# Kernel tuning notes

Hardware: AMD Instinct MI355X
Metric: run time of the kernel (lower is better)

## Reference

```python
import jax, jax.numpy as jnp
import numpy as np

B, D, C = 524288, 8, 32
EPS = 1e-4
DT, BETA, CLAMP, STEPS = 0.12, 1.0, 3.0, 4


def setup_inputs() -> dict:
    key = jax.random.key(0)
    k1, k2 = jax.random.split(key)
    z = jax.random.normal(k1, (B, D), dtype=jnp.float32)
    centers = jax.random.normal(k2, (C, D), dtype=jnp.float32) * 0.7
    mus = jnp.ones((C,), dtype=jnp.float32) * 0.4
    return {"z": z, "centers": centers, "mus": mus}


def reference(z, centers, mus):
    def grad_ln_n(z):
        # rvec: (B, C, D)
        rvec = z[:, None, :] - centers[None, :, :]
        r2 = jnp.sum(rvec * rvec, axis=-1) + EPS   # (B, C)
        r = jnp.sqrt(r2)
        n = 1.0 + jnp.sum(mus[None, :] / r, axis=-1)          # (B,)
        # g = sum_c -mu_c * rvec_c / (r_c * r2_c)
        g = -jnp.sum((mus[None, :] / (r * r2))[:, :, None] * rvec, axis=1)  # (B, D)
        return g / n[:, None]

    for _ in range(STEPS):
        z = jnp.clip(z + DT * BETA * grad_ln_n(z), -CLAMP, CLAMP)
    return z
```

## Files before the change

kernel.cpp:

```cpp
#include <hip/hip_runtime.h>
#include <stdint.h>

#define NB 524288
#define NC 32
#define EPSV 1e-4f
#define DTB 0.12f
#define CLAMPV 3.0f
#define NSTEPS 4

typedef float f32x16 __attribute__((ext_vector_type(16)));
typedef short short8 __attribute__((ext_vector_type(8)));

union FragU { uint32_t u[4]; short8 s; uint4 q; };

__device__ __forceinline__ uint32_t pkbf16(float a, float b) {
    uint32_t r;
    asm("v_cvt_pk_bf16_f32 %0, %1, %2" : "=v"(r) : "v"(a), "v"(b));
    return r;
}
__device__ __forceinline__ float lo16f(uint32_t w) { return __uint_as_float(w << 16); }
__device__ __forceinline__ float hi16f(uint32_t w) { return __uint_as_float(w & 0xffff0000u); }
__device__ __forceinline__ float sx32(float v) { return __shfl_xor(v, 32); }

__global__ void prep_kernel(const float* __restrict__ centers,
                            const float* __restrict__ mus,
                            uint4* __restrict__ wsu) {
    int t = threadIdx.x;
    if (t >= 64) return;
    int row = t & 31, part = t >> 5;

    float mu = mus[row];
    float im2 = 1.0f / (mu * mu);
    float c[8];
    float bb = EPSV;
    #pragma unroll
    for (int d = 0; d < 8; ++d) { c[d] = centers[row * 8 + d]; bb = fmaf(c[d], c[d], bb); }
    float v[8];
    #pragma unroll
    for (int i = 0; i < 8; ++i) {
        int k = part * 8 + i;
        v[i] = (k < 8) ? (-2.0f * c[k] * im2) : (k == 8) ? (bb * im2) : 0.0f;
    }
    uint32_t h[4], l[4];
    #pragma unroll
    for (int j = 0; j < 4; ++j) {
        float a = v[2 * j], b = v[2 * j + 1];
        h[j] = pkbf16(a, b);
        l[j] = pkbf16(a - lo16f(h[j]), b - hi16f(h[j]));
    }
    wsu[t]      = make_uint4(h[0], h[1], h[2], h[3]);
    wsu[64 + t] = make_uint4(l[0], l[1], l[2], l[3]);

    #pragma unroll
    for (int ch = 0; ch < 2; ++ch) {
        float v2[8];
        #pragma unroll
        for (int i = 0; i < 8; ++i) {
            int k = part * 8 + i;
            int within = (k & 3) + 8 * ((k >> 2) & 1) + 4 * (k >> 3);
            int ci = ch * 16 + within;
            float muc = mus[ci];
            float im2c = 1.0f / (muc * muc);
            v2[i] = (row < 8) ? (centers[ci * 8 + row] * im2c) : (row == 8) ? im2c : 0.0f;
        }
        uint32_t h2[4], l2[4];
        #pragma unroll
        for (int j = 0; j < 4; ++j) {
            float a = v2[2 * j], b = v2[2 * j + 1];
            h2[j] = pkbf16(a, b);
            l2[j] = pkbf16(a - lo16f(h2[j]), b - hi16f(h2[j]));
        }
        wsu[128 + ch * 64 + t] = make_uint4(h2[0], h2[1], h2[2], h2[3]);
        wsu[256 + ch * 64 + t] = make_uint4(l2[0], l2[1], l2[2], l2[3]);
    }

    if (t < 32) {
        int h2i = t >> 4, r = t & 15;
        int ci = (r & 3) + 8 * (r >> 2) + 4 * h2i;
        float muc = mus[ci];
        ((float*)wsu)[1536 + t] = 1.0f / (muc * muc);
    }
}

__global__ __launch_bounds__(256, 4) void pm_kernel(
    const float* __restrict__ z_in,
    const uint4* __restrict__ wsu,
    float* __restrict__ out)
{
    const int tid  = threadIdx.x;
    const int wid  = tid >> 6;
    const int lane = tid & 63;
    const int hi   = lane >> 5;
    const int col  = lane & 31;
    const int point = blockIdx.x * 128 + wid * 32 + col;

    FragU A1h, A1l, A2h0, A2h1, A2l0, A2l1;
    A1h.q  = wsu[lane];        A1l.q  = wsu[64 + lane];
    A2h0.q = wsu[128 + lane];  A2h1.q = wsu[192 + lane];
    A2l0.q = wsu[256 + lane];  A2l1.q = wsu[320 + lane];

    const float* imt = ((const float*)wsu) + 1536 + hi * 16;
    float imv[16];
    #pragma unroll
    for (int r = 0; r < 16; ++r) imv[r] = imt[r];

    const float4* zp4 = (const float4*)z_in;
    float4 hvec = zp4[(size_t)point * 2 + hi];
    float za0 = hvec.x, za1 = hvec.y, za2 = hvec.z, za3 = hvec.w;
    float zb0 = sx32(za0), zb1 = sx32(za1), zb2 = sx32(za2), zb3 = sx32(za3);

    #pragma unroll
    for (int s = 0; s < NSTEPS; ++s) {
        float zz = za0 * za0;
        zz = fmaf(za1, za1, zz); zz = fmaf(za2, za2, zz); zz = fmaf(za3, za3, zz);
        zz = fmaf(zb0, zb0, zz); zz = fmaf(zb1, zb1, zz);
        zz = fmaf(zb2, zb2, zz); zz = fmaf(zb3, zb3, zz);

        uint32_t w0 = pkbf16(za0, za1), w1 = pkbf16(za2, za3);
        uint32_t w2 = pkbf16(zb0, zb1), w3w = pkbf16(zb2, zb3);
        uint32_t q0 = pkbf16(1.0f, 0.0f);
        uint32_t w0l = pkbf16(za0 - lo16f(w0), za1 - hi16f(w0));
        uint32_t w1l = pkbf16(za2 - lo16f(w1), za3 - hi16f(w1));
        uint32_t w2l = pkbf16(zb0 - lo16f(w2), zb1 - hi16f(w2));
        uint32_t w3l = pkbf16(zb2 - lo16f(w3w), zb3 - hi16f(w3w));

        FragU B1h, B1l;
        B1h.u[0] = hi ? q0 : w0;   B1h.u[1] = hi ? 0u : w1;
        B1h.u[2] = hi ? 0u : w2;   B1h.u[3] = hi ? 0u : w3w;
        B1l.u[0] = hi ? 0u : w0l;  B1l.u[1] = hi ? 0u : w1l;
        B1l.u[2] = hi ? 0u : w2l;  B1l.u[3] = hi ? 0u : w3l;

        f32x16 D1 = {};
        D1 = __builtin_amdgcn_mfma_f32_32x32x16_bf16(A1h.s, B1h.s, D1, 0, 0, 0);
        D1 = __builtin_amdgcn_mfma_f32_32x32x16_bf16(A1h.s, B1l.s, D1, 0, 0, 0);
        D1 = __builtin_amdgcn_mfma_f32_32x32x16_bf16(A1l.s, B1h.s, D1, 0, 0, 0);
        D1 = __builtin_amdgcn_mfma_f32_32x32x16_bf16(A1l.s, B1l.s, D1, 0, 0, 0);

        float wv[16];
        #pragma unroll
        for (int r = 0; r < 16; ++r) {
            float r2 = fmaf(zz, imv[r], D1[r]);
            wv[r] = __builtin_amdgcn_rsqf(r2);
        }
        float t0 = wv[0] + wv[1],   t1 = wv[2] + wv[3],   t2 = wv[4] + wv[5],   t3 = wv[6] + wv[7];
        float t4 = wv[8] + wv[9],   t5 = wv[10] + wv[11], t6 = wv[12] + wv[13], t7 = wv[14] + wv[15];
        float n_half = ((t0 + t1) + (t2 + t3)) + ((t4 + t5) + (t6 + t7));
        float w3v[16];
        #pragma unroll
        for (int r = 0; r < 16; ++r) w3v[r] = (wv[r] * wv[r]) * wv[r];

        FragU B2c0h, B2c1h, B2c0l, B2c1l;
        #pragma unroll
        for (int j = 0; j < 4; ++j) {
            float a = w3v[2 * j], b = w3v[2 * j + 1];
            uint32_t ph = pkbf16(a, b);
            B2c0h.u[j] = ph;
            B2c0l.u[j] = pkbf16(a - lo16f(ph), b - hi16f(ph));
        }
        #pragma unroll
        for (int j = 0; j < 4; ++j) {
            float a = w3v[8 + 2 * j], b = w3v[8 + 2 * j + 1];
            uint32_t ph = pkbf16(a, b);
            B2c1h.u[j] = ph;
            B2c1l.u[j] = pkbf16(a - lo16f(ph), b - hi16f(ph));
        }

        f32x16 D2 = {};
        D2 = __builtin_amdgcn_mfma_f32_32x32x16_bf16(A2h0.s, B2c0h.s, D2, 0, 0, 0);
        D2 = __builtin_amdgcn_mfma_f32_32x32x16_bf16(A2h1.s, B2c1h.s, D2, 0, 0, 0);
        D2 = __builtin_amdgcn_mfma_f32_32x32x16_bf16(A2l0.s, B2c0h.s, D2, 0, 0, 0);
        D2 = __builtin_amdgcn_mfma_f32_32x32x16_bf16(A2l1.s, B2c1h.s, D2, 0, 0, 0);
        D2 = __builtin_amdgcn_mfma_f32_32x32x16_bf16(A2h0.s, B2c0l.s, D2, 0, 0, 0);
        D2 = __builtin_amdgcn_mfma_f32_32x32x16_bf16(A2h1.s, B2c1l.s, D2, 0, 0, 0);
        D2 = __builtin_amdgcn_mfma_f32_32x32x16_bf16(A2l0.s, B2c0l.s, D2, 0, 0, 0);
        D2 = __builtin_amdgcn_mfma_f32_32x32x16_bf16(A2l1.s, B2c1l.s, D2, 0, 0, 0);

        float n  = 1.0f + n_half + sx32(n_half);
        float swp = D2[4];
        float sw = swp + sx32(swp);
        float scale = DTB * __builtin_amdgcn_rcpf(n);

        float g0 = fmaf(-sw, za0, D2[0]);
        float g1 = fmaf(-sw, za1, D2[1]);
        float g2 = fmaf(-sw, za2, D2[2]);
        float g3 = fmaf(-sw, za3, D2[3]);
        za0 = fminf(fmaxf(fmaf(scale, g0, za0), -CLAMPV), CLAMPV);
        za1 = fminf(fmaxf(fmaf(scale, g1, za1), -CLAMPV), CLAMPV);
        za2 = fminf(fmaxf(fmaf(scale, g2, za2), -CLAMPV), CLAMPV);
        za3 = fminf(fmaxf(fmaf(scale, g3, za3), -CLAMPV), CLAMPV);
        zb0 = sx32(za0); zb1 = sx32(za1); zb2 = sx32(za2); zb3 = sx32(za3);
    }

    float4* op = (float4*)out;
    op[(size_t)point * 2 + hi] = make_float4(za0, za1, za2, za3);
}

extern "C" void kernel_launch(void* const* d_in, const int* in_sizes, int n_in,
                              void* d_out, int out_size, void* d_ws, size_t ws_size,
                              hipStream_t stream) {
    const float* z       = (const float*)d_in[0];
    const float* centers = (const float*)d_in[1];
    const float* mus     = (const float*)d_in[2];
    float* out           = (float*)d_out;
    uint4* wsu           = (uint4*)d_ws;

    prep_kernel<<<1, 64, 0, stream>>>(centers, mus, wsu);
    pm_kernel<<<NB / 128, 256, 0, stream>>>(z, wsu, out);
}
```

Measured before the change: 38.45 us.

## Pack hi/lo split terms into K dimension to halve first MFMA stage

The first distance matmul packs the bf16 high and low splits of z into the unused K lanes of a single B fragment. Matching A fragments (hi/lo of the centers) replace the constant-one row, so only two MFMAs are needed instead of four, and the |c|^2+eps bias moves to a per-row VGPR add. The second stage splits its eight MFMAs into two independent accumulators so the dependent chain is shorter, at the cost of extra adds and 16 more registers for the bias table.

```diff
diff --git a/kernel.cpp b/kernel.cpp
--- a/kernel.cpp
+++ b/kernel.cpp
@@ -20,6 +20,7 @@
 }
 __device__ __forceinline__ float lo16f(uint32_t w) { return __uint_as_float(w << 16); }
 __device__ __forceinline__ float hi16f(uint32_t w) { return __uint_as_float(w & 0xffff0000u); }
+__device__ __forceinline__ float bfh(float v) { return lo16f(pkbf16(v, v)); }
 __device__ __forceinline__ float sx32(float v) { return __shfl_xor(v, 32); }
 
 __global__ void prep_kernel(const float* __restrict__ centers,
@@ -29,27 +30,27 @@
     if (t >= 64) return;
     int row = t & 31, part = t >> 5;
 
-    float mu = mus[row];
-    float im2 = 1.0f / (mu * mu);
-    float c[8];
-    float bb = EPSV;
-    #pragma unroll
-    for (int d = 0; d < 8; ++d) { c[d] = centers[row * 8 + d]; bb = fmaf(c[d], c[d], bb); }
-    float v[8];
-    #pragma unroll
-    for (int i = 0; i < 8; ++i) {
-        int k = part * 8 + i;
-        v[i] = (k < 8) ? (-2.0f * c[k] * im2) : (k == 8) ? (bb * im2) : 0.0f;
-    }
-    uint32_t h[4], l[4];
-    #pragma unroll
-    for (int j = 0; j < 4; ++j) {
-        float a = v[2 * j], b = v[2 * j + 1];
-        h[j] = pkbf16(a, b);
-        l[j] = pkbf16(a - lo16f(h[j]), b - hi16f(h[j]));
-    }
-    wsu[t]      = make_uint4(h[0], h[1], h[2], h[3]);
-    wsu[64 + t] = make_uint4(l[0], l[1], l[2], l[3]);
+    {
+        float mu = mus[row];
+        float im2 = 1.0f / (mu * mu);
+        float vh[8], vl[8];
+        #pragma unroll
+        for (int d = 0; d < 8; ++d) {
+            float v = -2.0f * centers[row * 8 + d] * im2;
+            float h = bfh(v);
+            vh[d] = h;
+            vl[d] = v - h;
+        }
+        uint4 f1, f2;
+        const float* e1 = (part == 0) ? vh : vl;
+        const float* e2 = (part == 0) ? vl : vh;
+        f1.x = pkbf16(e1[0], e1[1]); f1.y = pkbf16(e1[2], e1[3]);
+        f1.z = pkbf16(e1[4], e1[5]); f1.w = pkbf16(e1[6], e1[7]);
+        f2.x = pkbf16(e2[0], e2[1]); f2.y = pkbf16(e2[2], e2[3]);
+        f2.z = pkbf16(e2[4], e2[5]); f2.w = pkbf16(e2[6], e2[7]);
+        wsu[t]      = f1;
+        wsu[64 + t] = f2;
+    }
 
     #pragma unroll
     for (int ch = 0; ch < 2; ++ch) {
@@ -78,7 +79,15 @@
         int h2i = t >> 4, r = t & 15;
         int ci = (r & 3) + 8 * (r >> 2) + 4 * h2i;
         float muc = mus[ci];
-        ((float*)wsu)[1536 + t] = 1.0f / (muc * muc);
+        float im2c = 1.0f / (muc * muc);
+        float bbc = EPSV;
+        #pragma unroll
+        for (int d = 0; d < 8; ++d) {
+            float cd = centers[ci * 8 + d];
+            bbc = fmaf(cd, cd, bbc);
+        }
+        ((float*)wsu)[1536 + t] = im2c;
+        ((float*)wsu)[1568 + t] = bbc * im2c;
     }
 }
 
@@ -94,15 +103,16 @@
     const int col  = lane & 31;
     const int point = blockIdx.x * 128 + wid * 32 + col;
 
-    FragU A1h, A1l, A2h0, A2h1, A2l0, A2l1;
-    A1h.q  = wsu[lane];        A1l.q  = wsu[64 + lane];
+    FragU A1f1, A1f2, A2h0, A2h1, A2l0, A2l1;
+    A1f1.q = wsu[lane];        A1f2.q = wsu[64 + lane];
     A2h0.q = wsu[128 + lane];  A2h1.q = wsu[192 + lane];
     A2l0.q = wsu[256 + lane];  A2l1.q = wsu[320 + lane];
 
     const float* imt = ((const float*)wsu) + 1536 + hi * 16;
-    float imv[16];
+    const float* bbp = ((const float*)wsu) + 1568 + hi * 16;
+    float imv[16], bbt[16];
     #pragma unroll
-    for (int r = 0; r < 16; ++r) imv[r] = imt[r];
+    for (int r = 0; r < 16; ++r) { imv[r] = imt[r]; bbt[r] = bbp[r]; }
 
     const float4* zp4 = (const float4*)z_in;
     float4 hvec = zp4[(size_t)point * 2 + hi];
@@ -116,30 +126,27 @@
         zz = fmaf(zb0, zb0, zz); zz = fmaf(zb1, zb1, zz);
         zz = fmaf(zb2, zb2, zz); zz = fmaf(zb3, zb3, zz);
 
-        uint32_t w0 = pkbf16(za0, za1), w1 = pkbf16(za2, za3);
-        uint32_t w2 = pkbf16(zb0, zb1), w3w = pkbf16(zb2, zb3);
-        uint32_t q0 = pkbf16(1.0f, 0.0f);
-        uint32_t w0l = pkbf16(za0 - lo16f(w0), za1 - hi16f(w0));
-        uint32_t w1l = pkbf16(za2 - lo16f(w1), za3 - hi16f(w1));
-        uint32_t w2l = pkbf16(zb0 - lo16f(w2), zb1 - hi16f(w2));
-        uint32_t w3l = pkbf16(zb2 - lo16f(w3w), zb3 - hi16f(w3w));
-
-        FragU B1h, B1l;
-        B1h.u[0] = hi ? q0 : w0;   B1h.u[1] = hi ? 0u : w1;
-        B1h.u[2] = hi ? 0u : w2;   B1h.u[3] = hi ? 0u : w3w;
-        B1l.u[0] = hi ? 0u : w0l;  B1l.u[1] = hi ? 0u : w1l;
-        B1l.u[2] = hi ? 0u : w2l;  B1l.u[3] = hi ? 0u : w3l;
+        uint32_t h0 = pkbf16(za0, za1), h1 = pkbf16(za2, za3);
+        uint32_t h2 = pkbf16(zb0, zb1), h3 = pkbf16(zb2, zb3);
+        uint32_t l0 = pkbf16(za0 - lo16f(h0), za1 - hi16f(h0));
+        uint32_t l1 = pkbf16(za2 - lo16f(h1), za3 - hi16f(h1));
+        uint32_t l2 = pkbf16(zb0 - lo16f(h2), zb1 - hi16f(h2));
+        uint32_t l3 = pkbf16(zb2 - lo16f(h3), zb3 - hi16f(h3));
+
+        FragU B1;
+        B1.u[0] = hi ? l2 : h0;
+        B1.u[1] = hi ? l3 : h1;
+        B1.u[2] = hi ? l0 : h2;
+        B1.u[3] = hi ? l1 : h3;
 
         f32x16 D1 = {};
-        D1 = __builtin_amdgcn_mfma_f32_32x32x16_bf16(A1h.s, B1h.s, D1, 0, 0, 0);
-        D1 = __builtin_amdgcn_mfma_f32_32x32x16_bf16(A1h.s, B1l.s, D1, 0, 0, 0);
-        D1 = __builtin_amdgcn_mfma_f32_32x32x16_bf16(A1l.s, B1h.s, D1, 0, 0, 0);
-        D1 = __builtin_amdgcn_mfma_f32_32x32x16_bf16(A1l.s, B1l.s, D1, 0, 0, 0);
+        D1 = __builtin_amdgcn_mfma_f32_32x32x16_bf16(A1f1.s, B1.s, D1, 0, 0, 0);
+        D1 = __builtin_amdgcn_mfma_f32_32x32x16_bf16(A1f2.s, B1.s, D1, 0, 0, 0);
 
         float wv[16];
         #pragma unroll
         for (int r = 0; r < 16; ++r) {
-            float r2 = fmaf(zz, imv[r], D1[r]);
+            float r2 = fmaf(zz, imv[r], D1[r] + bbt[r]);
             wv[r] = __builtin_amdgcn_rsqf(r2);
         }
         float t0 = wv[0] + wv[1],   t1 = wv[2] + wv[3],   t2 = wv[4] + wv[5],   t3 = wv[6] + wv[7];
@@ -165,25 +172,25 @@
             B2c1l.u[j] = pkbf16(a - lo16f(ph), b - hi16f(ph));
         }
 
-        f32x16 D2 = {};
-        D2 = __builtin_amdgcn_mfma_f32_32x32x16_bf16(A2h0.s, B2c0h.s, D2, 0, 0, 0);
-        D2 = __builtin_amdgcn_mfma_f32_32x32x16_bf16(A2h1.s, B2c1h.s, D2, 0, 0, 0);
-        D2 = __builtin_amdgcn_mfma_f32_32x32x16_bf16(A2l0.s, B2c0h.s, D2, 0, 0, 0);
-        D2 = __builtin_amdgcn_mfma_f32_32x32x16_bf16(A2l1.s, B2c1h.s, D2, 0, 0, 0);
-        D2 = __builtin_amdgcn_mfma_f32_32x32x16_bf16(A2h0.s, B2c0l.s, D2, 0, 0, 0);
-        D2 = __builtin_amdgcn_mfma_f32_32x32x16_bf16(A2h1.s, B2c1l.s, D2, 0, 0, 0);
-        D2 = __builtin_amdgcn_mfma_f32_32x32x16_bf16(A2l0.s, B2c0l.s, D2, 0, 0, 0);
-        D2 = __builtin_amdgcn_mfma_f32_32x32x16_bf16(A2l1.s, B2c1l.s, D2, 0, 0, 0);
+        f32x16 D2a = {}, D2b = {};
+        D2a = __builtin_amdgcn_mfma_f32_32x32x16_bf16(A2h0.s, B2c0h.s, D2a, 0, 0, 0);
+        D2b = __builtin_amdgcn_mfma_f32_32x32x16_bf16(A2h1.s, B2c1h.s, D2b, 0, 0, 0);
+        D2a = __builtin_amdgcn_mfma_f32_32x32x16_bf16(A2l0.s, B2c0h.s, D2a, 0, 0, 0);
+        D2b = __builtin_amdgcn_mfma_f32_32x32x16_bf16(A2l1.s, B2c1h.s, D2b, 0, 0, 0);
+        D2a = __builtin_amdgcn_mfma_f32_32x32x16_bf16(A2h0.s, B2c0l.s, D2a, 0, 0, 0);
+        D2b = __builtin_amdgcn_mfma_f32_32x32x16_bf16(A2h1.s, B2c1l.s, D2b, 0, 0, 0);
+        D2a = __builtin_amdgcn_mfma_f32_32x32x16_bf16(A2l0.s, B2c0l.s, D2a, 0, 0, 0);
+        D2b = __builtin_amdgcn_mfma_f32_32x32x16_bf16(A2l1.s, B2c1l.s, D2b, 0, 0, 0);
 
         float n  = 1.0f + n_half + sx32(n_half);
-        float swp = D2[4];
+        float swp = D2a[4] + D2b[4];
         float sw = swp + sx32(swp);
         float scale = DTB * __builtin_amdgcn_rcpf(n);
 
-        float g0 = fmaf(-sw, za0, D2[0]);
-        float g1 = fmaf(-sw, za1, D2[1]);
-        float g2 = fmaf(-sw, za2, D2[2]);
-        float g3 = fmaf(-sw, za3, D2[3]);
+        float g0 = fmaf(-sw, za0, D2a[0] + D2b[0]);
+        float g1 = fmaf(-sw, za1, D2a[1] + D2b[1]);
+        float g2 = fmaf(-sw, za2, D2a[2] + D2b[2]);
+        float g3 = fmaf(-sw, za3, D2a[3] + D2b[3]);
         za0 = fminf(fmaxf(fmaf(scale, g0, za0), -CLAMPV), CLAMPV);
         za1 = fminf(fmaxf(fmaf(scale, g1, za1), -CLAMPV), CLAMPV);
         za2 = fminf(fmaxf(fmaf(scale, g2, za2), -CLAMPV), CLAMPV);
```

Result: no change. 38.75 us (median of 3 runs) (+0.8%).
